# Kernel tuning notes

Hardware: AMD Instinct MI355X
Metric: run time of the kernel (lower is better)

Reference implementation:

```python
import jax, jax.numpy as jnp
import numpy as np

EPS = 1e-3  # Keras BatchNormalization default epsilon


def _bn(x, gamma, beta, mean, var):
    # inference batch norm, channels-last
    inv = gamma * jax.lax.rsqrt(var + EPS)
    return x * inv + (beta - mean * inv)


def setup_inputs() -> dict:
    key = jax.random.key(0)
    ks = jax.random.split(key, 13)
    B, D, H, W, C, F = 2, 48, 48, 48, 64, 128
    return {
        "x": jax.random.normal(ks[0], (B, D, H, W, C), dtype=jnp.float32),
        "dw_kernel": jax.random.normal(ks[1], (3, 3, 3, 1, C), dtype=jnp.float32) * 0.1,
        "dw_bias": jax.random.normal(ks[2], (C,), dtype=jnp.float32) * 0.1,
        "bn1_gamma": jax.random.uniform(ks[3], (C,), dtype=jnp.float32, minval=0.5, maxval=1.5),
        "bn1_beta": jax.random.normal(ks[4], (C,), dtype=jnp.float32) * 0.1,
        "bn1_mean": jax.random.normal(ks[5], (C,), dtype=jnp.float32) * 0.1,
        "bn1_var": jax.random.uniform(ks[6], (C,), dtype=jnp.float32, minval=0.5, maxval=1.5),
        "pw_kernel": jax.random.normal(ks[7], (C, F), dtype=jnp.float32) * 0.1,
        "pw_bias": jax.random.normal(ks[8], (F,), dtype=jnp.float32) * 0.1,
        "bn2_gamma": jax.random.uniform(ks[9], (F,), dtype=jnp.float32, minval=0.5, maxval=1.5),
        "bn2_beta": jax.random.normal(ks[10], (F,), dtype=jnp.float32) * 0.1,
        "bn2_mean": jax.random.normal(ks[11], (F,), dtype=jnp.float32) * 0.1,
        "bn2_var": jax.random.uniform(ks[12], (F,), dtype=jnp.float32, minval=0.5, maxval=1.5),
    }


def reference(x, dw_kernel, dw_bias, bn1_gamma, bn1_beta, bn1_mean, bn1_var,
              pw_kernel, pw_bias, bn2_gamma, bn2_beta, bn2_mean, bn2_var):
    C = x.shape[-1]
    # True depthwise conv3d (replaces the per-channel Python loop of Conv3D(1,...))
    y = jax.lax.conv_general_dilated(
        x, dw_kernel,
        window_strides=(1, 1, 1), padding="SAME",
        dimension_numbers=("NDHWC", "DHWIO", "NDHWC"),
        feature_group_count=C,
    ) + dw_bias
    y = jax.nn.relu(_bn(y, bn1_gamma, bn1_beta, bn1_mean, bn1_var))
    # pointwise 1x1x1 conv == channel GEMM
    z = jnp.einsum("bdhwc,cf->bdhwf", y, pw_kernel) + pw_bias
    z = jax.nn.relu(_bn(z, bn2_gamma, bn2_beta, bn2_mean, bn2_var))
    return z
```

## Files before the change

### kernel.cpp

```cpp
#include <hip/hip_runtime.h>
#include <hip/hip_bf16.h>

#define EPS 1e-3f

typedef __attribute__((ext_vector_type(8))) short short8;
typedef __attribute__((ext_vector_type(4))) float v4f;

__device__ __forceinline__ unsigned short f2bf(float f) {
    unsigned int u = __float_as_uint(f);
    unsigned int r = (u + 0x7fffu + ((u >> 16) & 1u)) >> 16;
    return (unsigned short)r;
}

__global__ __launch_bounds__(256) void prep_kernel(
    const float* __restrict__ dwb,
    const float* __restrict__ g1, const float* __restrict__ b1,
    const float* __restrict__ m1, const float* __restrict__ v1,
    const float* __restrict__ pw, const float* __restrict__ pwb,
    const float* __restrict__ g2, const float* __restrict__ b2,
    const float* __restrict__ m2, const float* __restrict__ v2,
    float* __restrict__ scale1, float* __restrict__ shift1,
    float* __restrict__ s2, float* __restrict__ t2,
    unsigned short* __restrict__ Wt)
{
    int tid = threadIdx.x;
    if (blockIdx.x == 0) {
        if (tid < 64) {
            float inv = g1[tid] * rsqrtf(v1[tid] + EPS);
            scale1[tid] = inv;
            shift1[tid] = dwb[tid] * inv + b1[tid] - m1[tid] * inv;
        }
        if (tid < 128) {
            float inv = g2[tid] * rsqrtf(v2[tid] + EPS);
            s2[tid] = inv;
            t2[tid] = pwb[tid] * inv + b2[tid] - m2[tid] * inv;
        }
    }
    int idx = blockIdx.x * 256 + tid;
    int j     = idx & 7;
    int lane  = (idx >> 3) & 63;
    int kstep = (idx >> 9) & 1;
    int ntile = idx >> 10;
    int k = kstep * 32 + (lane >> 4) * 8 + j;
    int f = ntile * 16 + (lane & 15);
    Wt[idx] = f2bf(pw[k * 128 + f]);
}

__global__ __launch_bounds__(256, 3) void fused_kernel(
    const float* __restrict__ x,
    const float* __restrict__ wgt,
    const float* __restrict__ scale1,
    const float* __restrict__ shift1,
    const unsigned short* __restrict__ Wt,
    const float* __restrict__ s2,
    const float* __restrict__ t2,
    float* __restrict__ out)
{
    __shared__ float wS[27 * 64];
    __shared__ float sS[64];
    __shared__ float tS[64];
    __shared__ float s2S[128];
    __shared__ float t2S[128];
    __shared__ unsigned short yS[64 * 72];

    int tid = threadIdx.x;
    for (int i = tid; i < 27 * 64; i += 256) wS[i] = wgt[i];
    if (tid < 64) { sS[tid] = scale1[tid]; tS[tid] = shift1[tid]; }
    if (tid < 128) { s2S[tid] = s2[tid]; t2S[tid] = t2[tid]; }
    __syncthreads();

    int n   = blockIdx.x;
    int g   = (n & 7) * 72 + (n >> 3);
    int bdg = g / 36;
    int hw  = g % 36;
    int b    = bdg >> 3;
    int dgrp = bdg & 7;
    int d0   = dgrp * 6;
    int w0  = (hw % 3) * 16;
    int h0  = (hw / 3) * 4;

    int tx = tid & 15;
    int ty = tid >> 4;
    int c0 = tx * 4;
    int wq = ty & 3;
    int rh = ty >> 2;

    int wv   = tid >> 6;
    int lane = tid & 63;
    int lrow = lane & 15;
    int quad = lane >> 4;

    int w0t = w0 + wq * 4;
    float mwL = (w0t >= 1)  ? 1.f : 0.f;
    float mwR = (w0t <= 43) ? 1.f : 0.f;
    int wcl[6];
    #pragma unroll
    for (int p = 0; p < 6; ++p)
        wcl[p] = min(max(w0t - 1 + p, 0), 47) * 64;

    int h = h0 + rh;
    bool hok[3];
    int  hcl[3];
    #pragma unroll
    for (int hh = 0; hh < 3; ++hh) {
        int zh = h + hh - 1;
        hok[hh] = (zh >= 0 && zh < 48);
        hcl[hh] = min(max(zh, 0), 47) * 48 * 64;
    }

    const long slab_stride = 48 * 48 * 64;

    float4 acc[3][4];
    #pragma unroll
    for (int a = 0; a < 3; ++a)
        #pragma unroll
        for (int r = 0; r < 4; ++r) acc[a][r] = make_float4(0.f, 0.f, 0.f, 0.f);

    #pragma unroll
    for (int k = 0; k < 8; ++k) {
        int s = d0 - 1 + k;
        bool s_ok = (s >= 0) && (s < 48);

        if (s_ok) {
            const float* dp = x + ((long)(b * 48 + s) * 48 * 48) * 64 + c0;
            #pragma unroll
            for (int hh = 0; hh < 3; ++hh) {
                if (hok[hh]) {
                    const float* rowp = dp + hcl[hh];
                    float4 xv[6];
                    #pragma unroll
                    for (int p = 0; p < 6; ++p)
                        xv[p] = *(const float4*)(rowp + wcl[p]);
                    xv[0].x *= mwL; xv[0].y *= mwL; xv[0].z *= mwL; xv[0].w *= mwL;
                    xv[5].x *= mwR; xv[5].y *= mwR; xv[5].z *= mwR; xv[5].w *= mwR;
                    #pragma unroll
                    for (int m = 0; m < 6; ++m) {
                        if (m >= k - 2 && m <= k) {
                            const int wz  = k - m;
                            const int aid = m % 3;
                            #pragma unroll
                            for (int ww = 0; ww < 3; ++ww) {
                                const float4 wvv = *(const float4*)(&wS[((wz * 3 + hh) * 3 + ww) * 64 + c0]);
                                #pragma unroll
                                for (int r = 0; r < 4; ++r) {
                                    acc[aid][r].x += xv[r + ww].x * wvv.x;
                                    acc[aid][r].y += xv[r + ww].y * wvv.y;
                                    acc[aid][r].z += xv[r + ww].z * wvv.z;
                                    acc[aid][r].w += xv[r + ww].w * wvv.w;
                                }
                            }
                        }
                    }
                }
            }
        }

        if (k >= 2) {
            const int m   = k - 2;
            const int aid = m % 3;

            __syncthreads();

            {
                float4 s1 = *(const float4*)(&sS[c0]);
                float4 t1 = *(const float4*)(&tS[c0]);
                #pragma unroll
                for (int r = 0; r < 4; ++r) {
                    ushort4 o;
                    o.x = f2bf(fmaxf(acc[aid][r].x * s1.x + t1.x, 0.f));
                    o.y = f2bf(fmaxf(acc[aid][r].y * s1.y + t1.y, 0.f));
                    o.z = f2bf(fmaxf(acc[aid][r].z * s1.z + t1.z, 0.f));
                    o.w = f2bf(fmaxf(acc[aid][r].w * s1.w + t1.w, 0.f));
                    *(ushort4*)(&yS[(ty * 4 + r) * 72 + c0]) = o;
                    acc[aid][r] = make_float4(0.f, 0.f, 0.f, 0.f);
                }
            }
            __syncthreads();

            const short8 a0 = *(const short8*)(&yS[(wv * 16 + lrow) * 72 + quad * 8]);
            const short8 a1 = *(const short8*)(&yS[(wv * 16 + lrow) * 72 + 32 + quad * 8]);

            v4f gacc[8];
            #pragma unroll
            for (int nn = 0; nn < 8; ++nn) gacc[nn] = (v4f){0.f, 0.f, 0.f, 0.f};

            #pragma unroll
            for (int nn = 0; nn < 8; ++nn) {
                short8 b0 = *(const short8*)(Wt + ((nn * 2 + 0) * 64 + lane) * 8);
                short8 b1 = *(const short8*)(Wt + ((nn * 2 + 1) * 64 + lane) * 8);
                gacc[nn] = __builtin_amdgcn_mfma_f32_16x16x32_bf16(a0, b0, gacc[nn], 0, 0, 0);
                gacc[nn] = __builtin_amdgcn_mfma_f32_16x16x32_bf16(a1, b1, gacc[nn], 0, 0, 0);
            }

            int d = d0 + m;
            long base_out = ((((long)b * 48 + d) * 48 + (h0 + wv)) * 48 + w0) * 128;
            #pragma unroll
            for (int nn = 0; nn < 8; ++nn) {
                int f = nn * 16 + lrow;
                float sf = s2S[f];
                float tf = t2S[f];
                #pragma unroll
                for (int r = 0; r < 4; ++r) {
                    float v = fmaxf(gacc[nn][r] * sf + tf, 0.f);
                    out[base_out + (quad * 4 + r) * 128 + f] = v;
                }
            }
        }
    }
}

extern "C" void kernel_launch(void* const* d_in, const int* in_sizes, int n_in,
                              void* d_out, int out_size, void* d_ws, size_t ws_size,
                              hipStream_t stream)
{
    const float* x   = (const float*)d_in[0];
    const float* dwk = (const float*)d_in[1];
    const float* dwb = (const float*)d_in[2];
    const float* g1  = (const float*)d_in[3];
    const float* b1  = (const float*)d_in[4];
    const float* m1  = (const float*)d_in[5];
    const float* v1  = (const float*)d_in[6];
    const float* pw  = (const float*)d_in[7];
    const float* pwb = (const float*)d_in[8];
    const float* g2  = (const float*)d_in[9];
    const float* b2  = (const float*)d_in[10];
    const float* m2  = (const float*)d_in[11];
    const float* v2  = (const float*)d_in[12];

    float* outp = (float*)d_out;

    float* scale1 = (float*)d_ws;
    float* shift1 = scale1 + 64;
    float* s2     = scale1 + 128;
    float* t2     = scale1 + 256;
    unsigned short* Wt = (unsigned short*)((char*)d_ws + 2048);

    hipLaunchKernelGGL(prep_kernel, dim3(32), dim3(256), 0, stream,
                       dwb, g1, b1, m1, v1, pw, pwb, g2, b2, m2, v2,
                       scale1, shift1, s2, t2, Wt);

    hipLaunchKernelGGL(fused_kernel, dim3(576), dim3(256), 0, stream,
                       x, dwk, scale1, shift1, Wt, s2, t2, outp);
}
```

Baseline: 205.5 us.

## Halve depth per block, double grid, and double-buffer the staging tile

Each block now handles 3 output depth slices instead of 6, which doubles the grid to 1152 blocks. The launch-bounds occupancy hint rises from 3 to 5 blocks per CU. The staging tile for the bf16 intermediate is double-buffered, so one of the two __syncthreads per slice can be dropped, and the accumulator ring indexing is simplified. The aim is more parallelism and better latency hiding. In exchange, the depth halo is re-read more often (5 slabs per 3 outputs instead of 8 per 6), and the tighter register budget may cause spills.

```diff
diff --git a/kernel.cpp b/kernel.cpp
--- a/kernel.cpp
+++ b/kernel.cpp
@@ -46,7 +46,7 @@
     Wt[idx] = f2bf(pw[k * 128 + f]);
 }
 
-__global__ __launch_bounds__(256, 3) void fused_kernel(
+__global__ __launch_bounds__(256, 5) void fused_kernel(
     const float* __restrict__ x,
     const float* __restrict__ wgt,
     const float* __restrict__ scale1,
@@ -61,7 +61,7 @@
     __shared__ float tS[64];
     __shared__ float s2S[128];
     __shared__ float t2S[128];
-    __shared__ unsigned short yS[64 * 72];
+    __shared__ unsigned short yS[2][64 * 72];
 
     int tid = threadIdx.x;
     for (int i = tid; i < 27 * 64; i += 256) wS[i] = wgt[i];
@@ -70,12 +70,12 @@
     __syncthreads();
 
     int n   = blockIdx.x;
-    int g   = (n & 7) * 72 + (n >> 3);
+    int g   = (n & 7) * 144 + (n >> 3);
     int bdg = g / 36;
     int hw  = g % 36;
-    int b    = bdg >> 3;
-    int dgrp = bdg & 7;
-    int d0   = dgrp * 6;
+    int b    = bdg >> 4;
+    int dgrp = bdg & 15;
+    int d0   = dgrp * 3;
     int w0  = (hw % 3) * 16;
     int h0  = (hw / 3) * 4;
 
@@ -108,8 +108,6 @@
         hcl[hh] = min(max(zh, 0), 47) * 48 * 64;
     }
 
-    const long slab_stride = 48 * 48 * 64;
-
     float4 acc[3][4];
     #pragma unroll
     for (int a = 0; a < 3; ++a)
@@ -117,7 +115,7 @@
         for (int r = 0; r < 4; ++r) acc[a][r] = make_float4(0.f, 0.f, 0.f, 0.f);
 
     #pragma unroll
-    for (int k = 0; k < 8; ++k) {
+    for (int k = 0; k < 5; ++k) {
         int s = d0 - 1 + k;
         bool s_ok = (s >= 0) && (s < 48);
 
@@ -134,19 +132,18 @@
                     xv[0].x *= mwL; xv[0].y *= mwL; xv[0].z *= mwL; xv[0].w *= mwL;
                     xv[5].x *= mwR; xv[5].y *= mwR; xv[5].z *= mwR; xv[5].w *= mwR;
                     #pragma unroll
-                    for (int m = 0; m < 6; ++m) {
+                    for (int m = 0; m < 3; ++m) {
                         if (m >= k - 2 && m <= k) {
-                            const int wz  = k - m;
-                            const int aid = m % 3;
+                            const int wz = k - m;
                             #pragma unroll
                             for (int ww = 0; ww < 3; ++ww) {
                                 const float4 wvv = *(const float4*)(&wS[((wz * 3 + hh) * 3 + ww) * 64 + c0]);
                                 #pragma unroll
                                 for (int r = 0; r < 4; ++r) {
-                                    acc[aid][r].x += xv[r + ww].x * wvv.x;
-                                    acc[aid][r].y += xv[r + ww].y * wvv.y;
-                                    acc[aid][r].z += xv[r + ww].z * wvv.z;
-                                    acc[aid][r].w += xv[r + ww].w * wvv.w;
+                                    acc[m][r].x += xv[r + ww].x * wvv.x;
+                                    acc[m][r].y += xv[r + ww].y * wvv.y;
+                                    acc[m][r].z += xv[r + ww].z * wvv.z;
+                                    acc[m][r].w += xv[r + ww].w * wvv.w;
                                 }
                             }
                         }
@@ -156,10 +153,8 @@
         }
 
         if (k >= 2) {
-            const int m   = k - 2;
-            const int aid = m % 3;
-
-            __syncthreads();
+            const int m = k - 2;
+            const int bu = m & 1;
 
             {
                 float4 s1 = *(const float4*)(&sS[c0]);
@@ -167,18 +162,17 @@
                 #pragma unroll
                 for (int r = 0; r < 4; ++r) {
                     ushort4 o;
-                    o.x = f2bf(fmaxf(acc[aid][r].x * s1.x + t1.x, 0.f));
-                    o.y = f2bf(fmaxf(acc[aid][r].y * s1.y + t1.y, 0.f));
-                    o.z = f2bf(fmaxf(acc[aid][r].z * s1.z + t1.z, 0.f));
-                    o.w = f2bf(fmaxf(acc[aid][r].w * s1.w + t1.w, 0.f));
-                    *(ushort4*)(&yS[(ty * 4 + r) * 72 + c0]) = o;
-                    acc[aid][r] = make_float4(0.f, 0.f, 0.f, 0.f);
+                    o.x = f2bf(fmaxf(acc[m][r].x * s1.x + t1.x, 0.f));
+                    o.y = f2bf(fmaxf(acc[m][r].y * s1.y + t1.y, 0.f));
+                    o.z = f2bf(fmaxf(acc[m][r].z * s1.z + t1.z, 0.f));
+                    o.w = f2bf(fmaxf(acc[m][r].w * s1.w + t1.w, 0.f));
+                    *(ushort4*)(&yS[bu][(ty * 4 + r) * 72 + c0]) = o;
                 }
             }
             __syncthreads();
 
-            const short8 a0 = *(const short8*)(&yS[(wv * 16 + lrow) * 72 + quad * 8]);
-            const short8 a1 = *(const short8*)(&yS[(wv * 16 + lrow) * 72 + 32 + quad * 8]);
+            const short8 a0 = *(const short8*)(&yS[bu][(wv * 16 + lrow) * 72 + quad * 8]);
+            const short8 a1 = *(const short8*)(&yS[bu][(wv * 16 + lrow) * 72 + 32 + quad * 8]);
 
             v4f gacc[8];
             #pragma unroll
@@ -239,6 +233,6 @@
                        dwb, g1, b1, m1, v1, pw, pwb, g2, b2, m2, v2,
                        scale1, shift1, s2, t2, Wt);
 
-    hipLaunchKernelGGL(fused_kernel, dim3(576), dim3(256), 0, stream,
+    hipLaunchKernelGGL(fused_kernel, dim3(1152), dim3(256), 0, stream,
                        x, dwk, scale1, shift1, Wt, s2, t2, outp);
 }
```

After: 296.2 us. 1.44x slower.
